# Performance work log

Hardware: AMD Instinct MI355X
Metric: run time of the kernel (lower is better)

Reference implementation:

```python
import jax, jax.numpy as jnp
import numpy as np

N_NODES = 50000
N_EDGES = 800000
N_GRAPHS = 256
N_IN = 300
HID_ATT = 128
NHID = 300
NOUT = 768
SLOPE = 0.2  # GATv2 default negative_slope


def _glorot(key, shape):
    fan_in, fan_out = shape[0], shape[-1]
    s = jnp.sqrt(2.0 / (fan_in + fan_out))
    return (jax.random.normal(key, shape, jnp.float32) * s).astype(jnp.float32)


def setup_inputs() -> dict:
    key = jax.random.key(0)
    ks = jax.random.split(key, 24)
    x = jax.random.normal(ks[0], (N_NODES, N_IN), jnp.float32)
    edge_index = jax.random.randint(ks[1], (2, N_EDGES), 0, N_NODES, jnp.int32)
    batch = jnp.sort(jax.random.randint(ks[2], (N_NODES,), 0, N_GRAPHS, jnp.int32))
    dims = [(N_IN, HID_ATT), (HID_ATT, HID_ATT), (HID_ATT, HID_ATT), (HID_ATT, NHID)]
    inp = {"x": x, "edge_index": edge_index, "batch": batch}
    ki = 3
    for l, (di, do) in enumerate(dims):
        inp[f"Wl{l}"] = _glorot(ks[ki], (di, do)); ki += 1
        inp[f"bl{l}"] = jnp.zeros((do,), jnp.float32)
        inp[f"Wr{l}"] = _glorot(ks[ki], (di, do)); ki += 1
        inp[f"br{l}"] = jnp.zeros((do,), jnp.float32)
        inp[f"att{l}"] = _glorot(ks[ki], (do, 1))[:, 0]; ki += 1
        inp[f"bias{l}"] = jnp.zeros((do,), jnp.float32)
    inp["fc1_W"] = _glorot(ks[ki], (NHID, NHID)); ki += 1
    inp["fc1_b"] = jnp.zeros((NHID,), jnp.float32)
    inp["fc2_W"] = _glorot(ks[ki], (NHID, NOUT)); ki += 1
    inp["fc2_b"] = jnp.zeros((NOUT,), jnp.float32)
    return inp


def _gatv2_layer(h, src, dst, Wl, bl, Wr, br, att, bias):
    # GATv2Conv, heads=1: alpha_ij = softmax_j( att . leaky_relu(Wl h_j + Wr h_i) ),
    # out_i = sum_j alpha_ij * (Wl h_j) + bias, softmax over incoming edges of i (dst).
    xl = h @ Wl + bl                         # [N, C] source transform
    xr = h @ Wr + br                         # [N, C] target transform
    m = xl[src] + xr[dst]                    # [E, C]
    e = jnp.where(m > 0, m, SLOPE * m)       # leaky_relu
    logits = e @ att                         # [E]
    mx = jax.ops.segment_max(logits, dst, num_segments=N_NODES)
    a = jnp.exp(logits - mx[dst])
    denom = jax.ops.segment_sum(a, dst, num_segments=N_NODES)
    alpha = a / denom[dst]                   # segment softmax (self-loops => no empty segs)
    out = jax.ops.segment_sum(xl[src] * alpha[:, None], dst, num_segments=N_NODES)
    return out + bias


def reference(x, edge_index, batch,
              Wl0, bl0, Wr0, br0, att0, bias0,
              Wl1, bl1, Wr1, br1, att1, bias1,
              Wl2, bl2, Wr2, br2, att2, bias2,
              Wl3, bl3, Wr3, br3, att3, bias3,
              fc1_W, fc1_b, fc2_W, fc2_b):
    loops = jnp.arange(N_NODES, dtype=edge_index.dtype)  # add_self_loops=True
    src = jnp.concatenate([edge_index[0], loops])
    dst = jnp.concatenate([edge_index[1], loops])
    layers = [(Wl0, bl0, Wr0, br0, att0, bias0),
              (Wl1, bl1, Wr1, br1, att1, bias1),
              (Wl2, bl2, Wr2, br2, att2, bias2),
              (Wl3, bl3, Wr3, br3, att3, bias3)]
    h = x
    for i, (Wl, bl, Wr, br, att, b) in enumerate(layers):
        h = _gatv2_layer(h, src, dst, Wl, bl, Wr, br, att, b)
        if i < len(layers) - 1:  # BasicGNN: act between layers, not after last
            h = jax.nn.relu(h)
    h = jax.nn.relu(h)  # encoder's relu after GAT
    # global_mean_pool
    s = jax.ops.segment_sum(h, batch, num_segments=N_GRAPHS)
    cnt = jax.ops.segment_sum(jnp.ones((N_NODES,), h.dtype), batch, num_segments=N_GRAPHS)
    g = s / jnp.maximum(cnt, 1.0)[:, None]   # [n_graphs, NHID]
    g = jax.nn.relu(g @ fc1_W + fc1_b)
    return g @ fc2_W + fc2_b                 # [n_graphs, NOUT]
```

## Files before the change

kernel.cpp:

```cpp
#include <hip/hip_runtime.h>
#include <hip/hip_bf16.h>
#include <math.h>

#define N_NODES 50000
#define N_EDGES 800000
#define E_TOT   (N_EDGES + N_NODES)
#define N_GRAPHS 256
#define SLOPE 0.2f
#define NB_SCAN ((N_NODES + 255) / 256)
#define NPANEL 782
#define WCOLS 768
#define POOL_SPLIT 8
#define HSTRIDE 304
#define XSTRIDE 320

typedef __attribute__((ext_vector_type(4))) float f32x4;
typedef _Float16 f16x2 __attribute__((ext_vector_type(2)));
typedef _Float16 f16x4 __attribute__((ext_vector_type(4)));
typedef _Float16 f16x8 __attribute__((ext_vector_type(8)));

__device__ __forceinline__ void gl_lds16(const void* g, void* l) {
  __builtin_amdgcn_global_load_lds(
      (const __attribute__((address_space(1))) unsigned int*)g,
      (__attribute__((address_space(3))) unsigned int*)l, 16, 0, 0);
}

__global__ void conv_x(const float* __restrict__ x, _Float16* __restrict__ A) {
  int id = blockIdx.x * blockDim.x + threadIdx.x;
  const int total = NPANEL * 64 * 40;
  if (id >= total) return;
  int kc = id % 40;
  int m  = (id / 40) % 64;
  int p  = id / 2560;
  int n = p * 64 + m;
  f16x8 hv;
#pragma unroll
  for (int i = 0; i < 8; ++i) {
    int k = kc * 8 + i;
    float v = (n < N_NODES && k < 300) ? x[(size_t)n * 300 + k] : 0.f;
    hv[i] = (_Float16)v;
  }
  size_t ce = (((size_t)p * 40 + kc) * 64 + m) * 8;
  *(f16x8*)&A[ce] = hv;
}

__global__ void conv_w_all(const float* __restrict__ W0l, const float* __restrict__ W0r,
                           const float* __restrict__ W1l, const float* __restrict__ W1r,
                           const float* __restrict__ W2l, const float* __restrict__ W2r,
                           const float* __restrict__ W3l, const float* __restrict__ W3r,
                           _Float16* __restrict__ W) {
  int id = blockIdx.x * blockDim.x + threadIdx.x;
  if (id >= 88 * WCOLS) return;
  int n = id % WCOLS, gkc = id / WCOLS;
  int l, kc;
  if (gkc < 40)      { l = 0; kc = gkc; }
  else if (gkc < 56) { l = 1; kc = gkc - 40; }
  else if (gkc < 72) { l = 2; kc = gkc - 56; }
  else               { l = 3; kc = gkc - 72; }
  const float* Wl = (l == 0) ? W0l : (l == 1) ? W1l : (l == 2) ? W2l : W3l;
  const float* Wr = (l == 0) ? W0r : (l == 1) ? W1r : (l == 2) ? W2r : W3r;
  int K = (l == 0) ? 300 : 128;
  int C = (l == 3) ? 300 : 128;
  int NL = (l == 3) ? 304 : 128;
  f16x8 hv;
#pragma unroll
  for (int i = 0; i < 8; ++i) {
    int k = kc * 8 + i;
    float v = 0.f;
    if (k < K) {
      if (n < NL) { if (n < C) v = Wl[(size_t)k * C + n]; }
      else if (n < 2 * NL && (n - NL) < C) v = Wr[(size_t)k * C + (n - NL)];
    }
    hv[i] = (_Float16)v;
  }
  *(f16x8*)&W[(size_t)id * 8] = hv;
}

__global__ void init_aux(const float* __restrict__ a0, const float* __restrict__ a1,
                         const float* __restrict__ a2, const float* __restrict__ a3,
                         f16x2* __restrict__ att_h, float* __restrict__ gpool) {
  int t = blockIdx.x * blockDim.x + threadIdx.x;
  if (t < 4 * 192) {
    int l = t / 192, i = t % 192;
    const float* a = (l == 0) ? a0 : (l == 1) ? a1 : (l == 2) ? a2 : a3;
    int C = (l == 3) ? 300 : 128;
    int c = 2 * i;
    f16x2 r;
    r[0] = (c < C) ? (_Float16)a[c] : (_Float16)0.f;
    r[1] = (c + 1 < C) ? (_Float16)a[c + 1] : (_Float16)0.f;
    att_h[t] = r;
  }
  int u = t - 768;
  if (u >= 0 && u < N_GRAPHS * 300) gpool[u] = 0.f;
}

__global__ __launch_bounds__(256, 2) void gemm_dual(
    const _Float16* __restrict__ A, const _Float16* __restrict__ W,
    const float* __restrict__ biasl, const float* __restrict__ biasr,
    _Float16* __restrict__ xlh, _Float16* __restrict__ xrh,
    int Kp, int C, int NL, int CSg) {
  __shared__ _Float16 As[4][64][8];
  __shared__ _Float16 Ws[4][256][8];
  const int tid = threadIdx.x, wv = tid >> 6, lane = tid & 63;
  const int p = blockIdx.x, n0 = blockIdx.y * 256;
  const int kcn = Kp >> 3, nk = Kp >> 5;
  const size_t abase0 = (size_t)p * kcn * 512;
  const int rsel = lane >> 4, rrow = lane & 15;
  f32x4 z4 = {0.f, 0.f, 0.f, 0.f};
  f32x4 acc[4][4];
#pragma unroll
  for (int a = 0; a < 4; ++a)
#pragma unroll
    for (int b = 0; b < 4; ++b) acc[a][b] = z4;

  for (int s = 0; s < nk; ++s) {
    const size_t abase = abase0 + (size_t)s * 2048;
    for (int q = wv; q < 20; q += 4) {
      const _Float16* g;
      _Float16* l;
      if (q < 4) {
        g = A + abase + q * 512;
        l = &As[0][0][0] + q * 512;
      } else {
        int j = q - 4;
        g = W + ((size_t)(s * 4 + (j >> 2)) * WCOLS + n0 + (j & 3) * 64) * 8;
        l = &Ws[0][0][0] + j * 512;
      }
      gl_lds16(g + lane * 8, l);
    }
    __syncthreads();
    f16x8 af[4], bf[4];
#pragma unroll
    for (int mt = 0; mt < 4; ++mt)
      af[mt] = *(const f16x8*)&As[rsel][mt * 16 + rrow][0];
#pragma unroll
    for (int nt = 0; nt < 4; ++nt)
      bf[nt] = *(const f16x8*)&Ws[rsel][wv * 64 + nt * 16 + rrow][0];
#pragma unroll
    for (int mt = 0; mt < 4; ++mt)
#pragma unroll
      for (int nt = 0; nt < 4; ++nt)
        acc[mt][nt] = __builtin_amdgcn_mfma_f32_16x16x32_f16(af[mt], bf[nt], acc[mt][nt], 0, 0, 0);
    __syncthreads();
  }
#pragma unroll
  for (int mt = 0; mt < 4; ++mt) {
    int r0 = p * 64 + mt * 16 + rsel * 4;
#pragma unroll
    for (int nt = 0; nt < 4; ++nt) {
      int gc = n0 + wv * 64 + nt * 16 + rrow;
#pragma unroll
      for (int j = 0; j < 4; ++j) {
        int row = r0 + j;
        if (row >= N_NODES) continue;
        float v = acc[mt][nt][j];
        if (gc < NL) {
          if (gc < C) xlh[(size_t)row * CSg + gc] = (_Float16)(v + biasl[gc]);
        } else {
          int c2 = gc - NL;
          if (c2 >= 0 && c2 < C) xrh[(size_t)row * CSg + c2] = (_Float16)(v + biasr[c2]);
        }
      }
    }
  }
}

__global__ void zero_ints(int* __restrict__ p, int n) {
  int i = blockIdx.x * blockDim.x + threadIdx.x;
  if (i < n) p[i] = 0;
}

__global__ void deg_count(const int* __restrict__ ei, int* __restrict__ deg) {
  int e = blockIdx.x * blockDim.x + threadIdx.x;
  if (e >= E_TOT) return;
  int d = (e < N_EDGES) ? ei[N_EDGES + e] : e - N_EDGES;
  atomicAdd(&deg[d], 1);
}

__global__ void scan1(const int* __restrict__ deg, int* __restrict__ rp,
                      int* __restrict__ bsum) {
  __shared__ int s[256];
  int i = blockIdx.x * 256 + threadIdx.x;
  int v = (i < N_NODES) ? deg[i] : 0;
  s[threadIdx.x] = v;
  __syncthreads();
  for (int off = 1; off < 256; off <<= 1) {
    int t = (threadIdx.x >= off) ? s[threadIdx.x - off] : 0;
    __syncthreads();
    s[threadIdx.x] += t;
    __syncthreads();
  }
  if (i < N_NODES) rp[i] = s[threadIdx.x] - v;
  if (threadIdx.x == 255) bsum[blockIdx.x] = s[255];
}

__global__ void scan2(int* __restrict__ bsum) {
  __shared__ int s[256];
  int v = (threadIdx.x < NB_SCAN) ? bsum[threadIdx.x] : 0;
  s[threadIdx.x] = v;
  __syncthreads();
  for (int off = 1; off < 256; off <<= 1) {
    int t = (threadIdx.x >= off) ? s[threadIdx.x - off] : 0;
    __syncthreads();
    s[threadIdx.x] += t;
    __syncthreads();
  }
  if (threadIdx.x < NB_SCAN) bsum[threadIdx.x] = s[threadIdx.x] - v;
}

__global__ void scan3(int* __restrict__ rp, const int* __restrict__ bsum,
                      int* __restrict__ cursor) {
  int i = blockIdx.x * 256 + threadIdx.x;
  if (i < N_NODES) {
    int v = rp[i] + bsum[blockIdx.x];
    rp[i] = v;
    cursor[i] = v;
  }
  if (i == 0) rp[N_NODES] = E_TOT;
}

__global__ void fill_csr(const int* __restrict__ ei, int* __restrict__ cursor,
                         int* __restrict__ csr_src) {
  int e = blockIdx.x * blockDim.x + threadIdx.x;
  if (e >= E_TOT) return;
  int s, d;
  if (e < N_EDGES) { s = ei[e]; d = ei[N_EDGES + e]; }
  else             { s = d = e - N_EDGES; }
  int pos = atomicAdd(&cursor[d], 1);
  csr_src[pos] = s;
}

__device__ __forceinline__ void load_row128(f16x2* dst, const _Float16* p) {
  f16x8 t = *(const f16x8*)p;
#pragma unroll
  for (int j = 0; j < 4; ++j) {
    f16x2 r; r[0] = t[2 * j]; r[1] = t[2 * j + 1]; dst[j] = r;
  }
}

__device__ __forceinline__ void load_row300(f16x2* dst, const _Float16* row, int li) {
  f16x8 a = *(const f16x8*)(row + 8 * li);
  f16x8 b = *(const f16x8*)(row + 128 + 8 * li);
  f16x4 c = *(const f16x4*)(row + 256 + 4 * li);
#pragma unroll
  for (int j = 0; j < 4; ++j) {
    f16x2 r; r[0] = a[2 * j]; r[1] = a[2 * j + 1]; dst[j] = r;
  }
#pragma unroll
  for (int j = 0; j < 4; ++j) {
    f16x2 r; r[0] = b[2 * j]; r[1] = b[2 * j + 1]; dst[4 + j] = r;
  }
  {
    f16x2 r; r[0] = c[0]; r[1] = c[1]; dst[8] = r;
    f16x2 r2; r2[0] = c[2]; r2[1] = c[3]; dst[9] = r2;
  }
}

__global__ __launch_bounds__(256) void gat128(
    const int* __restrict__ rowptr, const int* __restrict__ csr_src,
    const _Float16* __restrict__ xlh, const _Float16* __restrict__ xrh,
    const f16x2* __restrict__ att_h, const float* __restrict__ bias,
    _Float16* __restrict__ Hp) {
  int wid = (int)((blockIdx.x * (size_t)blockDim.x + threadIdx.x) >> 6);
  int lane = threadIdx.x & 63;
  if (wid >= N_NODES) return;
  const int g = lane >> 4, li = lane & 15;
  const int c0 = li * 8;
  int beg = rowptr[wid], end = rowptr[wid + 1];

  f16x2 xri[4], attc[4];
  load_row128(xri, xrh + (size_t)wid * 128 + c0);
#pragma unroll
  for (int j = 0; j < 4; ++j) attc[j] = att_h[(c0 >> 1) + j];

  float acc[8];
#pragma unroll
  for (int k = 0; k < 8; ++k) acc[k] = 0.f;
  float dsum = 0.f;
  const f16x2 slope2 = {(_Float16)SLOPE, (_Float16)SLOPE};

  int e = beg + g;
  f16x2 bufA[4], bufB[4];
  {
    int e0 = e < end ? e : end - 1;
    load_row128(bufA, xlh + (size_t)csr_src[e0] * 128 + c0);
  }
  {
    int e1 = e + 4 < end ? e + 4 : end - 1;
    load_row128(bufB, xlh + (size_t)csr_src[e1] * 128 + c0);
  }
  int nit = (end - beg + 3) >> 2;

  auto step = [&](f16x2* cur) {
    bool valid = e < end;
    float v = 0.f;
#pragma unroll
    for (int j = 0; j < 4; ++j) {
      f16x2 m2 = cur[j] + xri[j];
      f16x2 lr = __builtin_elementwise_max(m2, slope2 * m2);
#if __has_builtin(__builtin_amdgcn_fdot2)
      v = __builtin_amdgcn_fdot2(lr, attc[j], v, false);
#else
      v += (float)lr[0] * (float)attc[j][0] + (float)lr[1] * (float)attc[j][1];
#endif
    }
    v += __shfl_xor(v, 1);
    v += __shfl_xor(v, 2);
    v += __shfl_xor(v, 4);
    v += __shfl_xor(v, 8);
    float w = valid ? __expf(v) : 0.f;
    dsum += w;
#pragma unroll
    for (int j = 0; j < 4; ++j) {
      acc[2 * j]     += w * (float)cur[j][0];
      acc[2 * j + 1] += w * (float)cur[j][1];
    }
    if (e - g + 8 < end) {
      int en = e + 8; if (en > end - 1) en = end - 1;
      load_row128(cur, xlh + (size_t)csr_src[en] * 128 + c0);
    }
    e += 4;
  };
  for (int it = 0; it < nit; it += 2) {
    step(bufA);
    if (it + 1 < nit) step(bufB);
  }

#pragma unroll
  for (int k = 0; k < 8; ++k) {
    acc[k] += __shfl_xor(acc[k], 16);
    acc[k] += __shfl_xor(acc[k], 32);
  }
  dsum += __shfl_xor(dsum, 16);
  dsum += __shfl_xor(dsum, 32);
  if (g != 0) return;
  float inv = 1.f / dsum;
  f16x8 hv;
#pragma unroll
  for (int k = 0; k < 8; ++k) {
    float vv = fmaxf(acc[k] * inv + bias[c0 + k], 0.f);
    hv[k] = (_Float16)vv;
  }
  int p = wid >> 6, mrow = wid & 63;
  size_t ce = (((size_t)p * 16 + li) * 64 + mrow) * 8;
  *(f16x8*)&Hp[ce] = hv;
}

__global__ __launch_bounds__(256) void gat300(
    const int* __restrict__ rowptr, const int* __restrict__ csr_src,
    const _Float16* __restrict__ xlh, const _Float16* __restrict__ xrh,
    const f16x2* __restrict__ att_h, const float* __restrict__ bias,
    _Float16* __restrict__ hout) {
  int wid = (int)((blockIdx.x * (size_t)blockDim.x + threadIdx.x) >> 6);
  int lane = threadIdx.x & 63;
  if (wid >= N_NODES) return;
  const int g = lane >> 4, li = lane & 15;
  int beg = rowptr[wid], end = rowptr[wid + 1];

  f16x2 xri[10], attc[10];
  load_row300(xri, xrh + (size_t)wid * XSTRIDE, li);
#pragma unroll
  for (int j = 0; j < 4; ++j) attc[j] = att_h[4 * li + j];
#pragma unroll
  for (int j = 0; j < 4; ++j) attc[4 + j] = att_h[64 + 4 * li + j];
  attc[8] = att_h[128 + 2 * li];
  attc[9] = att_h[128 + 2 * li + 1];

  float acc[20];
#pragma unroll
  for (int k = 0; k < 20; ++k) acc[k] = 0.f;
  float dsum = 0.f;
  const f16x2 slope2 = {(_Float16)SLOPE, (_Float16)SLOPE};

  int e = beg + g;
  f16x2 nxt[10];
  {
    int s = csr_src[e < end ? e : end - 1];
    load_row300(nxt, xlh + (size_t)s * XSTRIDE, li);
  }
  int nit = (end - beg + 3) >> 2;
  for (int it = 0; it < nit; ++it) {
    f16x2 cur[10];
#pragma unroll
    for (int j = 0; j < 10; ++j) cur[j] = nxt[j];
    bool valid = e < end;
    if (beg + (it + 1) * 4 < end) {
      int en = e + 4;
      int s = csr_src[en < end ? en : end - 1];
      load_row300(nxt, xlh + (size_t)s * XSTRIDE, li);
    }
    float v = 0.f;
#pragma unroll
    for (int j = 0; j < 10; ++j) {
      f16x2 m2 = cur[j] + xri[j];
      f16x2 lr = __builtin_elementwise_max(m2, slope2 * m2);
#if __has_builtin(__builtin_amdgcn_fdot2)
      v = __builtin_amdgcn_fdot2(lr, attc[j], v, false);
#else
      v += (float)lr[0] * (float)attc[j][0] + (float)lr[1] * (float)attc[j][1];
#endif
    }
    v += __shfl_xor(v, 1);
    v += __shfl_xor(v, 2);
    v += __shfl_xor(v, 4);
    v += __shfl_xor(v, 8);
    float w = valid ? __expf(v) : 0.f;
    dsum += w;
#pragma unroll
    for (int j = 0; j < 10; ++j) {
      acc[2 * j]     += w * (float)cur[j][0];
      acc[2 * j + 1] += w * (float)cur[j][1];
    }
    e += 4;
  }
#pragma unroll
  for (int k = 0; k < 20; ++k) {
    acc[k] += __shfl_xor(acc[k], 16);
    acc[k] += __shfl_xor(acc[k], 32);
  }
  dsum += __shfl_xor(dsum, 16);
  dsum += __shfl_xor(dsum, 32);
  if (g != 0) return;
  float inv = 1.f / dsum;
  f16x8 h1, h2;
  f16x4 h3;
#pragma unroll
  for (int k = 0; k < 8; ++k)
    h1[k] = (_Float16)fmaxf(acc[k] * inv + bias[8 * li + k], 0.f);
#pragma unroll
  for (int k = 0; k < 8; ++k)
    h2[k] = (_Float16)fmaxf(acc[8 + k] * inv + bias[128 + 8 * li + k], 0.f);
  if (li <= 10) {
#pragma unroll
    for (int k = 0; k < 4; ++k)
      h3[k] = (_Float16)fmaxf(acc[16 + k] * inv + bias[256 + 4 * li + k], 0.f);
  }
  _Float16* hr = hout + (size_t)wid * HSTRIDE;
  *(f16x8*)(hr + 8 * li) = h1;
  *(f16x8*)(hr + 128 + 8 * li) = h2;
  if (li <= 10) *(f16x4*)(hr + 256 + 4 * li) = h3;
}

__device__ int lower_bound_dev(const int* a, int n, int v) {
  int lo = 0, hi = n;
  while (lo < hi) { int mid = (lo + hi) >> 1; if (a[mid] < v) lo = mid + 1; else hi = mid; }
  return lo;
}

__global__ void pool_sum(const _Float16* __restrict__ h, const int* __restrict__ batch,
                         float* __restrict__ gsum) {
  int gi = blockIdx.x;
  int sp = blockIdx.y;
  int c = threadIdx.x;
  if (c >= 300) return;
  int start = lower_bound_dev(batch, N_NODES, gi);
  int end   = lower_bound_dev(batch, N_NODES, gi + 1);
  int len = end - start;
  int chunk = (len + POOL_SPLIT - 1) / POOL_SPLIT;
  int a = start + sp * chunk;
  int b = a + chunk; if (b > end) b = end;
  if (a >= b) return;
  float s0 = 0.f, s1 = 0.f, s2 = 0.f, s3 = 0.f;
  int n = a;
  for (; n + 3 < b; n += 4) {
    s0 += (float)h[(size_t)n * HSTRIDE + c];
    s1 += (float)h[(size_t)(n + 1) * HSTRIDE + c];
    s2 += (float)h[(size_t)(n + 2) * HSTRIDE + c];
    s3 += (float)h[(size_t)(n + 3) * HSTRIDE + c];
  }
  for (; n < b; ++n) s0 += (float)h[(size_t)n * HSTRIDE + c];
  atomicAdd(&gsum[(size_t)gi * 300 + c], (s0 + s1) + (s2 + s3));
}

__global__ void fc_kernel(const float* __restrict__ g, const float* __restrict__ W,
                          const float* __restrict__ b, float* __restrict__ out,
                          const int* __restrict__ batch,
                          int K, int N, int do_relu, int do_div) {
  __shared__ float row[304];
  int gi = blockIdx.x;
  float scale = 1.f;
  if (do_div) {
    int start = lower_bound_dev(batch, N_NODES, gi);
    int end   = lower_bound_dev(batch, N_NODES, gi + 1);
    int cnt = end - start;
    scale = 1.f / (float)(cnt > 0 ? cnt : 1);
  }
  for (int k = threadIdx.x; k < K; k += blockDim.x) row[k] = g[(size_t)gi * K + k] * scale;
  __syncthreads();
  int c = threadIdx.x;
  if (c >= N) return;
  float s = b[c];
  for (int k = 0; k < K; ++k) s += row[k] * W[(size_t)k * N + c];
  if (do_relu) s = fmaxf(s, 0.f);
  out[(size_t)gi * N + c] = s;
}

extern "C" void kernel_launch(void* const* d_in, const int* in_sizes, int n_in,
                              void* d_out, int out_size, void* d_ws, size_t ws_size,
                              hipStream_t stream) {
  const float* x     = (const float*)d_in[0];
  const int*   ei    = (const int*)d_in[1];
  const int*   batch = (const int*)d_in[2];
  const float* Wl[4], *bl[4], *Wr[4], *br[4], *att[4], *bias[4];
  for (int l = 0; l < 4; ++l) {
    Wl[l]   = (const float*)d_in[3 + l * 6 + 0];
    bl[l]   = (const float*)d_in[3 + l * 6 + 1];
    Wr[l]   = (const float*)d_in[3 + l * 6 + 2];
    br[l]   = (const float*)d_in[3 + l * 6 + 3];
    att[l]  = (const float*)d_in[3 + l * 6 + 4];
    bias[l] = (const float*)d_in[3 + l * 6 + 5];
  }
  const float* fc1_W = (const float*)d_in[27];
  const float* fc1_b = (const float*)d_in[28];
  const float* fc2_W = (const float*)d_in[29];
  const float* fc2_b = (const float*)d_in[30];

  char* wsb = (char*)d_ws;
  size_t off = 0;
  auto alloc = [&](size_t bytes) {
    void* p = (void*)(wsb + off);
    off += (bytes + 63) & ~(size_t)63;
    return p;
  };
  _Float16* xlh = (_Float16*)alloc((size_t)N_NODES * XSTRIDE * 2 + 128);
  _Float16* xrh = (_Float16*)alloc((size_t)N_NODES * XSTRIDE * 2 + 128);
  _Float16* A0  = (_Float16*)alloc((size_t)NPANEL * 40 * 512 * 2);
  _Float16* Hp  = (_Float16*)alloc((size_t)NPANEL * 16 * 512 * 2);
  _Float16* hbuf = (_Float16*)alloc((size_t)N_NODES * HSTRIDE * 2);
  float* gpool  = (float*)alloc((size_t)N_GRAPHS * 300 * 4);
  float* g1     = (float*)alloc((size_t)N_GRAPHS * 300 * 4);
  f16x2* att_h  = (f16x2*)alloc((size_t)4 * 192 * 4);
  _Float16* Wbuf = (_Float16*)alloc((size_t)88 * WCOLS * 8 * 2);
  const int Cdim[4] = {128, 128, 128, 300};
  const int NLv[4]  = {128, 128, 128, 304};
  const int Kpv[4]  = {320, 128, 128, 128};
  const int CSg[4]  = {128, 128, 128, XSTRIDE};
  const int Wbase[4] = {0, 40, 56, 72};
  int* deg     = (int*)alloc((size_t)N_NODES * 4);
  int* rowptr  = (int*)alloc((size_t)(N_NODES + 1) * 4);
  int* bsum    = (int*)alloc(256 * 4);
  int* cursor  = (int*)alloc((size_t)N_NODES * 4);
  int* csr_src = (int*)alloc((size_t)E_TOT * 4);

  conv_x<<<(NPANEL * 64 * 40 + 255) / 256, 256, 0, stream>>>(x, A0);
  conv_w_all<<<(88 * WCOLS + 255) / 256, 256, 0, stream>>>(
      Wl[0], Wr[0], Wl[1], Wr[1], Wl[2], Wr[2], Wl[3], Wr[3], Wbuf);
  init_aux<<<(768 + N_GRAPHS * 300 + 255) / 256, 256, 0, stream>>>(
      att[0], att[1], att[2], att[3], att_h, gpool);

  zero_ints<<<(N_NODES + 255) / 256, 256, 0, stream>>>(deg, N_NODES);
  deg_count<<<(E_TOT + 255) / 256, 256, 0, stream>>>(ei, deg);
  scan1<<<NB_SCAN, 256, 0, stream>>>(deg, rowptr, bsum);
  scan2<<<1, 256, 0, stream>>>(bsum);
  scan3<<<NB_SCAN, 256, 0, stream>>>(rowptr, bsum, cursor);
  fill_csr<<<(E_TOT + 255) / 256, 256, 0, stream>>>(ei, cursor, csr_src);

  const int nwave_blocks = (N_NODES + 3) / 4;
  for (int l = 0; l < 4; ++l) {
    const _Float16* Ain = (l == 0) ? A0 : Hp;
    const _Float16* Wp = Wbuf + (size_t)Wbase[l] * WCOLS * 8;
    int ny = (2 * NLv[l] + 255) / 256;
    dim3 gg(NPANEL, ny);
    gemm_dual<<<gg, 256, 0, stream>>>(Ain, Wp, bl[l], br[l],
                                      xlh, xrh, Kpv[l], Cdim[l], NLv[l], CSg[l]);
    if (l < 3) {
      gat128<<<nwave_blocks, 256, 0, stream>>>(
          rowptr, csr_src, xlh, xrh, att_h + l * 192, bias[l], Hp);
    } else {
      gat300<<<nwave_blocks, 256, 0, stream>>>(
          rowptr, csr_src, xlh, xrh, att_h + l * 192, bias[l], hbuf);
    }
  }
  {
    dim3 pg(N_GRAPHS, POOL_SPLIT);
    pool_sum<<<pg, 320, 0, stream>>>(hbuf, batch, gpool);
  }
  fc_kernel<<<N_GRAPHS, 320, 0, stream>>>(gpool, fc1_W, fc1_b, g1, batch, 300, 300, 1, 1);
  fc_kernel<<<N_GRAPHS, 768, 0, stream>>>(g1, fc2_W, fc2_b, (float*)d_out, batch, 300, 768, 0, 0);
}
```

Before: 547.7 us.

## Process 8 edges per wave with 16 channels per lane in gat128

```diff
diff --git a/kernel.cpp b/kernel.cpp
--- a/kernel.cpp
+++ b/kernel.cpp
@@ -230,11 +230,16 @@
   csr_src[pos] = s;
 }
 
-__device__ __forceinline__ void load_row128(f16x2* dst, const _Float16* p) {
-  f16x8 t = *(const f16x8*)p;
+__device__ __forceinline__ void load_row128w(f16x2* dst, const _Float16* p) {
+  f16x8 a = *(const f16x8*)p;
+  f16x8 b = *(const f16x8*)(p + 8);
 #pragma unroll
   for (int j = 0; j < 4; ++j) {
-    f16x2 r; r[0] = t[2 * j]; r[1] = t[2 * j + 1]; dst[j] = r;
+    f16x2 r; r[0] = a[2 * j]; r[1] = a[2 * j + 1]; dst[j] = r;
+  }
+#pragma unroll
+  for (int j = 0; j < 4; ++j) {
+    f16x2 r; r[0] = b[2 * j]; r[1] = b[2 * j + 1]; dst[4 + j] = r;
   }
 }
 
@@ -264,38 +269,40 @@
   int wid = (int)((blockIdx.x * (size_t)blockDim.x + threadIdx.x) >> 6);
   int lane = threadIdx.x & 63;
   if (wid >= N_NODES) return;
-  const int g = lane >> 4, li = lane & 15;
-  const int c0 = li * 8;
+  const int g = lane >> 3, li = lane & 7;
+  const int c0 = li * 16;
   int beg = rowptr[wid], end = rowptr[wid + 1];
 
-  f16x2 xri[4], attc[4];
-  load_row128(xri, xrh + (size_t)wid * 128 + c0);
-#pragma unroll
-  for (int j = 0; j < 4; ++j) attc[j] = att_h[(c0 >> 1) + j];
-
-  float acc[8];
-#pragma unroll
-  for (int k = 0; k < 8; ++k) acc[k] = 0.f;
+  f16x2 xri[8], attc[8];
+  load_row128w(xri, xrh + (size_t)wid * 128 + c0);
+#pragma unroll
+  for (int j = 0; j < 8; ++j) attc[j] = att_h[(c0 >> 1) + j];
+
+  float acc[16];
+#pragma unroll
+  for (int k = 0; k < 16; ++k) acc[k] = 0.f;
   float dsum = 0.f;
   const f16x2 slope2 = {(_Float16)SLOPE, (_Float16)SLOPE};
 
   int e = beg + g;
-  f16x2 bufA[4], bufB[4];
+  f16x2 nxt[8];
   {
     int e0 = e < end ? e : end - 1;
-    load_row128(bufA, xlh + (size_t)csr_src[e0] * 128 + c0);
-  }
-  {
-    int e1 = e + 4 < end ? e + 4 : end - 1;
-    load_row128(bufB, xlh + (size_t)csr_src[e1] * 128 + c0);
-  }
-  int nit = (end - beg + 3) >> 2;
-
-  auto step = [&](f16x2* cur) {
+    load_row128w(nxt, xlh + (size_t)csr_src[e0] * 128 + c0);
+  }
+  int nit = (end - beg + 7) >> 3;
+  for (int it = 0; it < nit; ++it) {
+    f16x2 cur[8];
+#pragma unroll
+    for (int j = 0; j < 8; ++j) cur[j] = nxt[j];
     bool valid = e < end;
+    if (beg + (it + 1) * 8 < end) {
+      int en = e + 8; if (en > end - 1) en = end - 1;
+      load_row128w(nxt, xlh + (size_t)csr_src[en] * 128 + c0);
+    }
     float v = 0.f;
 #pragma unroll
-    for (int j = 0; j < 4; ++j) {
+    for (int j = 0; j < 8; ++j) {
       f16x2 m2 = cur[j] + xri[j];
       f16x2 lr = __builtin_elementwise_max(m2, slope2 * m2);
 #if __has_builtin(__builtin_amdgcn_fdot2)
@@ -307,43 +314,38 @@
     v += __shfl_xor(v, 1);
     v += __shfl_xor(v, 2);
     v += __shfl_xor(v, 4);
-    v += __shfl_xor(v, 8);
     float w = valid ? __expf(v) : 0.f;
     dsum += w;
 #pragma unroll
-    for (int j = 0; j < 4; ++j) {
+    for (int j = 0; j < 8; ++j) {
       acc[2 * j]     += w * (float)cur[j][0];
       acc[2 * j + 1] += w * (float)cur[j][1];
     }
-    if (e - g + 8 < end) {
-      int en = e + 8; if (en > end - 1) en = end - 1;
-      load_row128(cur, xlh + (size_t)csr_src[en] * 128 + c0);
-    }
-    e += 4;
-  };
-  for (int it = 0; it < nit; it += 2) {
-    step(bufA);
-    if (it + 1 < nit) step(bufB);
-  }
-
-#pragma unroll
-  for (int k = 0; k < 8; ++k) {
+    e += 8;
+  }
+#pragma unroll
+  for (int k = 0; k < 16; ++k) {
+    acc[k] += __shfl_xor(acc[k], 8);
     acc[k] += __shfl_xor(acc[k], 16);
     acc[k] += __shfl_xor(acc[k], 32);
   }
+  dsum += __shfl_xor(dsum, 8);
   dsum += __shfl_xor(dsum, 16);
   dsum += __shfl_xor(dsum, 32);
   if (g != 0) return;
   float inv = 1.f / dsum;
-  f16x8 hv;
-#pragma unroll
-  for (int k = 0; k < 8; ++k) {
-    float vv = fmaxf(acc[k] * inv + bias[c0 + k], 0.f);
-    hv[k] = (_Float16)vv;
-  }
+  f16x8 hv1, hv2;
+#pragma unroll
+  for (int k = 0; k < 8; ++k)
+    hv1[k] = (_Float16)fmaxf(acc[k] * inv + bias[c0 + k], 0.f);
+#pragma unroll
+  for (int k = 0; k < 8; ++k)
+    hv2[k] = (_Float16)fmaxf(acc[8 + k] * inv + bias[c0 + 8 + k], 0.f);
   int p = wid >> 6, mrow = wid & 63;
-  size_t ce = (((size_t)p * 16 + li) * 64 + mrow) * 8;
-  *(f16x8*)&Hp[ce] = hv;
+  size_t ce1 = (((size_t)p * 16 + 2 * li) * 64 + mrow) * 8;
+  size_t ce2 = (((size_t)p * 16 + 2 * li + 1) * 64 + mrow) * 8;
+  *(f16x8*)&Hp[ce1] = hv1;
+  *(f16x8*)&Hp[ce2] = hv2;
 }
 
 __global__ __launch_bounds__(256) void gat300(
```

New measurement: 564.9 us. +3.1%, slower.
